# Optimization experiments

Hardware: AMD Instinct MI355X
Metric: run time of the kernel (lower is better)

The kernel has to match this reference:

```python
import jax, jax.numpy as jnp
import numpy as np
import math

B, C, L = 8, 128, 8192
MODES = 512
TIME_DIM = 256
HIDDEN = 352  # SwiGLU: int(2*4*128/3)=341 rounded up to multiple of 16
EPS = 1e-6


def setup_inputs() -> dict:
    key = jax.random.key(0)
    ks = jax.random.split(key, 16)
    scale = 1.0 / (C * C)
    return {
        "x": jax.random.normal(ks[0], (B, C, L), jnp.float32),
        "t_emb": jax.random.normal(ks[1], (B, TIME_DIM), jnp.float32),
        "w_real": scale * jax.random.normal(ks[2], (C, C, MODES), jnp.float32),
        "w_imag": scale * jax.random.normal(ks[3], (C, C, MODES), jnp.float32),
        "shifts": 0.05 * jax.random.normal(ks[4], (C,), jnp.float32),
        "pw_w": jax.random.normal(ks[5], (C, C), jnp.float32) / math.sqrt(C),
        "pw_b": jnp.zeros((C,), jnp.float32),
        "dw_w": jax.random.normal(ks[6], (C, 3), jnp.float32) / math.sqrt(3.0),
        "dw_b": jnp.zeros((C,), jnp.float32),
        "norm_w": jnp.ones((C,), jnp.float32),
        "w1": jax.random.normal(ks[7], (HIDDEN, C), jnp.float32) / math.sqrt(C),
        "w2": jax.random.normal(ks[8], (HIDDEN, C), jnp.float32) / math.sqrt(C),
        "w3": jax.random.normal(ks[9], (C, HIDDEN), jnp.float32) / math.sqrt(HIDDEN),
        "tw": jax.random.normal(ks[10], (C, TIME_DIM), jnp.float32) / math.sqrt(TIME_DIM),
        "tb": jnp.zeros((C,), jnp.float32),
    }


def reference(x, t_emb, w_real, w_imag, shifts, pw_w, pw_b, dw_w, dw_b,
              norm_w, w1, w2, w3, tw, tb):
    Lx = x.shape[-1]
    nfreq = Lx // 2 + 1
    k = min(MODES, nfreq)
    residual = x

    # --- spectral path ---
    x_ft = jnp.fft.rfft(x, axis=-1)  # (B,C,nfreq) complex64
    w = (w_real + 1j * w_imag)[:, :, :k]  # (C,O,modes)
    w_spec = jnp.einsum('bcm,com->bom', x_ft[:, :, :k], w)
    # SpectralRoPE phase rotation
    freqs = jnp.arange(MODES, dtype=jnp.float32)[:k]
    theta = -2.0 * jnp.pi * shifts[:, None] * freqs[None, :]  # (C,k)
    rot = jnp.exp(1j * theta)
    w_spec = w_spec * rot[None]
    out_ft = jnp.concatenate([w_spec, x_ft[:, :, k:]], axis=-1) if nfreq > k else w_spec
    global_out = jnp.fft.irfft(out_ft, n=Lx, axis=-1)

    # --- local path: pointwise (1x1) + depthwise (k=3, pad=1) conv ---
    pw = jnp.einsum('bcl,oc->bol', x, pw_w) + pw_b[None, :, None]
    xp = jnp.pad(x, ((0, 0), (0, 0), (1, 1)))
    dw = (dw_w[None, :, 0:1] * xp[:, :, :-2]
          + dw_w[None, :, 1:2] * xp[:, :, 1:-1]
          + dw_w[None, :, 2:3] * xp[:, :, 2:]) + dw_b[None, :, None]
    h = global_out + pw + dw

    # --- time bias ---
    t_bias = jax.nn.silu(t_emb) @ tw.T + tb  # (B,C)
    h = h + t_bias[:, :, None]

    # --- RMSNorm + SwiGLU over channel dim ---
    h = h.transpose(0, 2, 1)  # (B,L,C)
    h = h * jax.lax.rsqrt(jnp.mean(h * h, axis=-1, keepdims=True) + EPS)
    h = h * norm_w
    h = (jax.nn.silu(h @ w1.T) * (h @ w2.T)) @ w3.T
    h = h.transpose(0, 2, 1)  # (B,C,L)
    return h + residual
```

## Files before the change

### kernel.cpp

```cpp
#include <hip/hip_runtime.h>
#include <hip/hip_bf16.h>
#include <math.h>

typedef short short8 __attribute__((ext_vector_type(8)));
typedef short short4v __attribute__((ext_vector_type(4)));
typedef float f32x4 __attribute__((ext_vector_type(4)));
typedef __bf16 bf16x8 __attribute__((ext_vector_type(8)));

#define DEVI __device__ __forceinline__

DEVI float bf2f(short u) {
  union { unsigned int u32; float f; } c;
  c.u32 = ((unsigned int)(unsigned short)u) << 16;
  return c.f;
}
DEVI short f2bf(float f) {
  __hip_bfloat16 h = __float2bfloat16(f);
  unsigned short u;
  __builtin_memcpy(&u, &h, 2);
  return (short)u;
}
DEVI f32x4 mfma16(bf16x8 a, bf16x8 b, f32x4 c) {
  return __builtin_amdgcn_mfma_f32_16x16x32_bf16(a, b, c, 0, 0, 0);
}

#define GLL16(gsrc, ldst) __builtin_amdgcn_global_load_lds( \
    (__attribute__((address_space(1))) void*)(gsrc), \
    (__attribute__((address_space(3))) void*)(ldst), 16, 0, 0)

__global__ __launch_bounds__(256) void k_prep_x(const float* __restrict__ x,
                                                short* __restrict__ xbf,
                                                short* __restrict__ xT) {
  __shared__ short T[64][66];
  int t = threadIdx.x;
  int lt = blockIdx.x & 127;
  int ct = (blockIdx.x >> 7) & 1;
  int b  = blockIdx.x >> 8;
  int c0 = ct << 6, l0 = lt << 6;
  int i = t >> 2, j4 = (t & 3) << 4;
  const float* src = x + (size_t)(b * 128 + c0 + i) * 8192 + l0 + j4;
  short hv[16];
#pragma unroll
  for (int e = 0; e < 16; e += 4) {
    float4 v = *(const float4*)(src + e);
    hv[e] = f2bf(v.x); hv[e + 1] = f2bf(v.y); hv[e + 2] = f2bf(v.z); hv[e + 3] = f2bf(v.w);
  }
  short8 o0, o1;
#pragma unroll
  for (int e = 0; e < 8; ++e) { o0[e] = hv[e]; o1[e] = hv[8 + e]; }
  short* dst = xbf + (size_t)(b * 128 + c0 + i) * 8192 + l0 + j4;
  *(short8*)dst = o0;
  *(short8*)(dst + 8) = o1;
#pragma unroll
  for (int e = 0; e < 16; ++e) T[i][j4 + e] = hv[e];
  __syncthreads();
  int jj = t >> 2, i4 = (t & 3) << 4;
  short8 p0, p1;
#pragma unroll
  for (int e = 0; e < 8; ++e) { p0[e] = T[i4 + e][jj]; p1[e] = T[i4 + 8 + e][jj]; }
  short* d2 = xT + ((size_t)b * 8192 + l0 + jj) * 128 + c0 + i4;
  *(short8*)d2 = p0;
  *(short8*)(d2 + 8) = p1;
}

__global__ __launch_bounds__(256) void k_prep_tf(short* __restrict__ tf) {
  int n = blockIdx.x >> 2;
  int l0 = ((blockIdx.x & 3) << 11) + (threadIdx.x << 3);
  int m = n >> 1;
  int odd = n & 1;
  short8 o;
#pragma unroll
  for (int e = 0; e < 8; ++e) {
    int l = l0 + e;
    int r = (m * l) & 8191;
    float s, c;
    sincospif((float)r * (1.0f / 4096.0f), &s, &c);
    o[e] = f2bf(odd ? -s : c);
  }
  *(short8*)(tf + (size_t)n * 8192 + l0) = o;
}

__global__ __launch_bounds__(256) void k_prep_ti(short* __restrict__ ti) {
  int l = blockIdx.x;
  int k0 = threadIdx.x << 2;
  short4v o;
#pragma unroll
  for (int e = 0; e < 4; ++e) {
    int k = k0 + e;
    int m = (k < 512) ? k : (k - 512);
    int r = (m * l) & 8191;
    float s, c;
    sincospif((float)r * (1.0f / 4096.0f), &s, &c);
    o[e] = f2bf((k < 512) ? c : s);
  }
  *(short4v*)(ti + (size_t)l * 1024 + k0) = o;
}

__global__ __launch_bounds__(256) void k_prep_w(const float* __restrict__ w1,
                                                const float* __restrict__ w2,
                                                const float* __restrict__ w3,
                                                const float* __restrict__ pw_w,
                                                short* __restrict__ w12f,
                                                short* __restrict__ w3f,
                                                short* __restrict__ pwb) {
  int idx = blockIdx.x * 256 + threadIdx.x;
  if (idx < 98304) {
    int e = idx & 7, lane = (idx >> 3) & 63, ks = (idx >> 9) & 3, nt = idx >> 11;
    int rowk = lane & 15, kg = lane >> 4;
    int n = nt * 16 + rowk;
    int k = ks * 32 + kg * 8 + e;
    float v = 0.f;
    if (n < 352) v = w1[n * 128 + k];
    else if (n >= 384 && n < 736) v = w2[(n - 384) * 128 + k];
    w12f[idx] = f2bf(v);
  } else if (idx < 147456) {
    int q = idx - 98304;
    int e = q & 7, lane = (q >> 3) & 63;
    int rest = q >> 9;
    int nt = rest / 12, ks = rest - nt * 12;
    int rowk = lane & 15, kg = lane >> 4;
    int n = nt * 16 + rowk;
    int k = ks * 32 + kg * 8 + e;
    w3f[q] = f2bf(k < 352 ? w3[n * 352 + k] : 0.f);
  } else if (idx < 163840) {
    int q = idx - 147456;
    pwb[q] = f2bf(pw_w[q]);
  }
}

__global__ __launch_bounds__(256) void k_prep_bias(const float* __restrict__ t_emb,
                                                   const float* __restrict__ tw,
                                                   const float* __restrict__ tb,
                                                   const float* __restrict__ pw_b,
                                                   const float* __restrict__ dw_b,
                                                   float* __restrict__ bias) {
  __shared__ float s[256];
  int b = blockIdx.x, t = threadIdx.x;
  float v = t_emb[b * 256 + t];
  s[t] = v / (1.0f + __expf(-v));
  __syncthreads();
  if (t < 128) {
    float acc = tb[t] + pw_b[t] + dw_b[t];
    for (int j = 0; j < 256; ++j) acc += s[j] * tw[t * 256 + j];
    bias[b * 128 + t] = acc;
  }
}

__global__ __launch_bounds__(256) void k_zero(float4* __restrict__ p, int n4) {
  int i = blockIdx.x * 256 + threadIdx.x;
  if (i < n4) p[i] = make_float4(0.f, 0.f, 0.f, 0.f);
}

__global__ __launch_bounds__(256, 2) void k_fwd(const short* __restrict__ A,
                                                const short* __restrict__ Bt,
                                                float* __restrict__ X) {
  __shared__ short As[2][4096];
  __shared__ short Bs[2][4096];
  int t = threadIdx.x;
  int nt = blockIdx.x & 7;
  int mt = (blockIdx.x >> 3) & 7;
  int kc = blockIdx.x >> 6;
  int lane = t & 63, wv = t >> 6;
  int wr = wv >> 1, wc = wv & 1;

  int rA = t >> 2, g = t & 3;
  int gs0 = (g ^ ((rA >> 1) & 3)) << 3;
  int rB = rA + 64;
  int gs1 = (g ^ ((rB >> 1) & 3)) << 3;

  const short* aS0 = A + (size_t)(mt * 128 + rA) * 8192 + kc * 1024 + gs0;
  const short* aS1 = A + (size_t)(mt * 128 + rB) * 8192 + kc * 1024 + gs1;
  const short* bS0 = Bt + (size_t)(nt * 128 + rA) * 8192 + kc * 1024 + gs0;
  const short* bS1 = Bt + (size_t)(nt * 128 + rB) * 8192 + kc * 1024 + gs1;

  f32x4 acc[4][4];
#pragma unroll
  for (int i = 0; i < 4; ++i)
#pragma unroll
    for (int j = 0; j < 4; ++j) acc[i][j] = (f32x4){0.f, 0.f, 0.f, 0.f};

  GLL16(aS0, &As[0][t * 8]);
  GLL16(aS1, &As[0][2048 + t * 8]);
  GLL16(bS0, &Bs[0][t * 8]);
  GLL16(bS1, &Bs[0][2048 + t * 8]);

  int rowk = lane & 15, kg = lane >> 4;

  for (int ks = 0; ks < 32; ++ks) {
    __syncthreads();
    int buf = ks & 1;
    if (ks + 1 < 32) {
      int ko = (ks + 1) * 32;
      GLL16(aS0 + ko, &As[buf ^ 1][t * 8]);
      GLL16(aS1 + ko, &As[buf ^ 1][2048 + t * 8]);
      GLL16(bS0 + ko, &Bs[buf ^ 1][t * 8]);
      GLL16(bS1 + ko, &Bs[buf ^ 1][2048 + t * 8]);
    }
    bf16x8 af[4], bfr[4];
#pragma unroll
    for (int fr = 0; fr < 4; ++fr) {
      int rr = wr * 64 + fr * 16 + rowk;
      int gg = kg ^ ((rr >> 1) & 3);
      af[fr] = *(const bf16x8*)(&As[buf][rr * 32 + gg * 8]);
    }
#pragma unroll
    for (int fc = 0; fc < 4; ++fc) {
      int rr = wc * 64 + fc * 16 + rowk;
      int gg = kg ^ ((rr >> 1) & 3);
      bfr[fc] = *(const bf16x8*)(&Bs[buf][rr * 32 + gg * 8]);
    }
#pragma unroll
    for (int fr = 0; fr < 4; ++fr)
#pragma unroll
      for (int fc = 0; fc < 4; ++fc)
        acc[fr][fc] = mfma16(af[fr], bfr[fc], acc[fr][fc]);
  }

  int rbase = mt * 128 + wr * 64 + (lane >> 4) * 4;
  int cbase = nt * 128 + wc * 64 + (lane & 15);
#pragma unroll
  for (int fr = 0; fr < 4; ++fr)
#pragma unroll
    for (int fc = 0; fc < 4; ++fc)
#pragma unroll
      for (int j = 0; j < 4; ++j)
        unsafeAtomicAdd(&X[(size_t)(rbase + fr * 16 + j) * 1024 + cbase + fc * 16],
                        acc[fr][fc][j]);
}

__global__ __launch_bounds__(512) void k_spec(const float* __restrict__ X,
                                              const float* __restrict__ wre,
                                              const float* __restrict__ wim,
                                              const float* __restrict__ shifts,
                                              short* __restrict__ D) {
  __shared__ float red[16][256];
  int t = threadIdx.x;
  int tt = t & 255;
  int ch = t >> 8;
  int mt = blockIdx.x & 31, ot = blockIdx.x >> 5;
  int m = mt * 16 + (tt & 15);
  int o = ot * 16 + (tt >> 4);
  float ar[8], ai[8];
#pragma unroll
  for (int b = 0; b < 8; ++b) { ar[b] = 0.f; ai[b] = 0.f; }
  int cb = ch * 64;
  const float* wrp = wre + (size_t)(cb * 128 + o) * 512 + m;
  const float* wip = wim + (size_t)(cb * 128 + o) * 512 + m;
  const float* Xp = X + 2 * m;
#pragma unroll 4
  for (int cc = 0; cc < 64; ++cc) {
    float wr = wrp[(size_t)cc * 65536];
    float wi = wip[(size_t)cc * 65536];
    int c = cb + cc;
#pragma unroll
    for (int b = 0; b < 8; ++b) {
      float2 xv = *(const float2*)(Xp + (size_t)(b * 128 + c) * 1024);
      ar[b] += xv.x * wr - xv.y * wi;
      ai[b] += xv.x * wi + xv.y * wr;
    }
  }
  if (ch) {
#pragma unroll
    for (int b = 0; b < 8; ++b) { red[b * 2][tt] = ar[b]; red[b * 2 + 1][tt] = ai[b]; }
  }
  __syncthreads();
  if (!ch) {
#pragma unroll
    for (int b = 0; b < 8; ++b) { ar[b] += red[b * 2][tt]; ai[b] += red[b * 2 + 1][tt]; }
    float phi = -6.283185307179586f * shifts[o] * (float)m;
    float sp, cp;
    sincosf(phi, &sp, &cp);
    float sc = (m == 0 ? 1.0f : 2.0f) * (1.0f / 8192.0f);
#pragma unroll
    for (int b = 0; b < 8; ++b) {
      float yr = ar[b] * cp - ai[b] * sp;
      float yi = ar[b] * sp + ai[b] * cp;
      float2 xo = *(const float2*)(X + (size_t)(b * 128 + o) * 1024 + 2 * m);
      D[((size_t)b * 128 + o) * 1024 + m]       = f2bf(sc * (yr - xo.x));
      D[((size_t)b * 128 + o) * 1024 + 512 + m] = f2bf(-sc * (yi - xo.y));
    }
  }
}

__global__ __launch_bounds__(256, 2) void k_inv(const short* __restrict__ Ti,
                                                const short* __restrict__ D,
                                                const short* __restrict__ xT,
                                                const short* __restrict__ pwb,
                                                const float* __restrict__ dww,
                                                const float* __restrict__ bias,
                                                const float* __restrict__ nw,
                                                short* __restrict__ hn) {
  __shared__ short Sm[16384];
  __shared__ short xedge[256];
  __shared__ float rsS[2][128];
  short* As = Sm;
  short* Bs = Sm + 8192;
  int t = threadIdx.x;
  int lt = blockIdx.x & 63;
  int b  = blockIdx.x >> 6;
  int l0 = lt << 7;
  int lane = t & 63, wv = t >> 6;
  int wr = wv >> 1, wc = wv & 1;

  int rA = t >> 2, g = t & 3;
  int gs0 = (g ^ ((rA >> 1) & 3)) << 3;
  int rB = rA + 64;
  int gs1 = (g ^ ((rB >> 1) & 3)) << 3;

  const short* a1_0 = Ti + (size_t)(l0 + rA) * 1024 + gs0;
  const short* a1_1 = Ti + (size_t)(l0 + rB) * 1024 + gs1;
  const short* b1_0 = D + (size_t)(b * 128 + rA) * 1024 + gs0;
  const short* b1_1 = D + (size_t)(b * 128 + rB) * 1024 + gs1;
  const short* a2_0 = xT + ((size_t)b * 8192 + l0 + rA) * 128 + gs0;
  const short* a2_1 = xT + ((size_t)b * 8192 + l0 + rB) * 128 + gs1;
  const short* b2_0 = pwb + rA * 128 + gs0;
  const short* b2_1 = pwb + rB * 128 + gs1;

  f32x4 acc[4][4];
#pragma unroll
  for (int i = 0; i < 4; ++i)
#pragma unroll
    for (int j = 0; j < 4; ++j) acc[i][j] = (f32x4){0.f, 0.f, 0.f, 0.f};

  auto stage = [&](int buf, int ks) {
    int bo = buf * 4096;
    if (ks < 32) {
      int ko = ks * 32;
      GLL16(a1_0 + ko, &As[bo + t * 8]);
      GLL16(a1_1 + ko, &As[bo + 2048 + t * 8]);
      GLL16(b1_0 + ko, &Bs[bo + t * 8]);
      GLL16(b1_1 + ko, &Bs[bo + 2048 + t * 8]);
    } else {
      int ko = (ks - 32) * 32;
      GLL16(a2_0 + ko, &As[bo + t * 8]);
      GLL16(a2_1 + ko, &As[bo + 2048 + t * 8]);
      GLL16(b2_0 + ko, &Bs[bo + t * 8]);
      GLL16(b2_1 + ko, &Bs[bo + 2048 + t * 8]);
    }
  };

  stage(0, 0);
  int rowk = lane & 15, kg = lane >> 4;
  for (int ks = 0; ks < 36; ++ks) {
    __syncthreads();
    int buf = ks & 1;
    if (ks + 1 < 36) stage(buf ^ 1, ks + 1);
    bf16x8 af[4], bfr[4];
#pragma unroll
    for (int fr = 0; fr < 4; ++fr) {
      int rr = wr * 64 + fr * 16 + rowk;
      int gg = kg ^ ((rr >> 1) & 3);
      af[fr] = *(const bf16x8*)(&As[buf * 4096 + rr * 32 + gg * 8]);
    }
#pragma unroll
    for (int fc = 0; fc < 4; ++fc) {
      int rr = wc * 64 + fc * 16 + rowk;
      int gg = kg ^ ((rr >> 1) & 3);
      bfr[fc] = *(const bf16x8*)(&Bs[buf * 4096 + rr * 32 + gg * 8]);
    }
#pragma unroll
    for (int fr = 0; fr < 4; ++fr)
#pragma unroll
      for (int fc = 0; fc < 4; ++fc)
        acc[fr][fc] = mfma16(af[fr], bfr[fc], acc[fr][fc]);
  }

  __syncthreads();
  for (int i = t; i < 2080; i += 256) {
    if (i < 2048) {
      int row = i >> 4, seg = i & 15;
      short8 v = *(const short8*)(xT + ((size_t)b * 8192 + l0 + row) * 128 + seg * 8);
      *(short8*)(&Sm[row * 128 + seg * 8]) = v;
    } else {
      int e2 = i - 2048;
      int which = e2 >> 4, seg = e2 & 15;
      int l = which ? (l0 + 128) : (l0 - 1);
      short8 v = {0, 0, 0, 0, 0, 0, 0, 0};
      if (l >= 0 && l < 8192)
        v = *(const short8*)(xT + ((size_t)b * 8192 + l) * 128 + seg * 8);
      *(short8*)(&xedge[which * 128 + seg * 8]) = v;
    }
  }
  __syncthreads();

  const float* bb = bias + b * 128;
#pragma unroll
  for (int fc = 0; fc < 4; ++fc) {
    int o = wc * 64 + fc * 16 + rowk;
    float w0 = dww[o * 3], w1v = dww[o * 3 + 1], w2v = dww[o * 3 + 2];
    float bo = bb[o];
#pragma unroll
    for (int fr = 0; fr < 4; ++fr) {
#pragma unroll
      for (int j = 0; j < 4; ++j) {
        int ll = wr * 64 + fr * 16 + kg * 4 + j;
        float xm = (ll == 0)   ? bf2f(xedge[o])       : bf2f(Sm[(ll - 1) * 128 + o]);
        float x0 = bf2f(Sm[ll * 128 + o]);
        float xp = (ll == 127) ? bf2f(xedge[128 + o]) : bf2f(Sm[(ll + 1) * 128 + o]);
        acc[fr][fc][j] += w0 * xm + w1v * x0 + w2v * xp + bo + x0;
      }
    }
  }
#pragma unroll
  for (int fr = 0; fr < 4; ++fr) {
#pragma unroll
    for (int j = 0; j < 4; ++j) {
      float s = 0.f;
#pragma unroll
      for (int fc = 0; fc < 4; ++fc) { float v = acc[fr][fc][j]; s += v * v; }
      s += __shfl_xor(s, 1);
      s += __shfl_xor(s, 2);
      s += __shfl_xor(s, 4);
      s += __shfl_xor(s, 8);
      if (rowk == 0) rsS[wc][wr * 64 + fr * 16 + kg * 4 + j] = s;
    }
  }
  __syncthreads();
#pragma unroll
  for (int fr = 0; fr < 4; ++fr) {
#pragma unroll
    for (int j = 0; j < 4; ++j) {
      int ll = wr * 64 + fr * 16 + kg * 4 + j;
      float rms = rsqrtf((rsS[0][ll] + rsS[1][ll]) * (1.0f / 128.0f) + 1e-6f);
#pragma unroll
      for (int fc = 0; fc < 4; ++fc) {
        int o = wc * 64 + fc * 16 + rowk;
        hn[((size_t)b * 8192 + l0 + ll) * 128 + o] = f2bf(acc[fr][fc][j] * rms * nw[o]);
      }
    }
  }
}

__global__ __launch_bounds__(512, 2) void k_swi(const short* __restrict__ hn,
                                                const short* __restrict__ w12f,
                                                const short* __restrict__ w3f,
                                                const float* __restrict__ x,
                                                float* __restrict__ out) {
  __shared__ short smem[32768];
  short* hA = smem;
  short* uA = smem + 8192;
  float* tr = (float*)smem;

  int t = threadIdx.x;
  int lane = t & 63, wv = t >> 6;
  int rb = blockIdx.x;
  int bb_ = rb >> 7;
  int l0 = (rb & 127) << 6;
  size_t row0 = (size_t)rb * 64;

#pragma unroll
  for (int c = 0; c < 2; ++c) {
    int sidx = (wv * 2 + c) * 512 + lane * 8;
    int row = sidx >> 7;
    int g = (sidx >> 3) & 15;
    const short* src = hn + (row0 + row) * 128 + (g ^ (row & 7)) * 8;
    GLL16(src, &hA[sidx]);
  }
  __syncthreads();

  int wr = wv >> 2, wq = wv & 3;
  int rowk = lane & 15, kg = lane >> 4;

  f32x4 acc1[2][6], acc2[2][6];
#pragma unroll
  for (int i = 0; i < 2; ++i)
#pragma unroll
    for (int j = 0; j < 6; ++j) {
      acc1[i][j] = (f32x4){0.f, 0.f, 0.f, 0.f};
      acc2[i][j] = (f32x4){0.f, 0.f, 0.f, 0.f};
    }
#pragma unroll
  for (int ks = 0; ks < 4; ++ks) {
    bf16x8 a[2];
#pragma unroll
    for (int fr = 0; fr < 2; ++fr) {
      int rr = wr * 32 + fr * 16 + rowk;
      int gg = (ks * 4 + kg) ^ (rr & 7);
      a[fr] = *(const bf16x8*)(&hA[rr * 128 + gg * 8]);
    }
#pragma unroll
    for (int fc = 0; fc < 6; ++fc) {
      int nt = wq * 6 + fc;
      bf16x8 b1 = *(const bf16x8*)(w12f + ((size_t)(nt * 4 + ks) * 64 + lane) * 8);
      bf16x8 b2 = *(const bf16x8*)(w12f + ((size_t)((nt + 24) * 4 + ks) * 64 + lane) * 8);
#pragma unroll
      for (int fr = 0; fr < 2; ++fr) {
        acc1[fr][fc] = mfma16(a[fr], b1, acc1[fr][fc]);
        acc2[fr][fc] = mfma16(a[fr], b2, acc2[fr][fc]);
      }
    }
  }
#pragma unroll
  for (int fr = 0; fr < 2; ++fr)
#pragma unroll
    for (int fc = 0; fc < 6; ++fc)
#pragma unroll
      for (int j = 0; j < 4; ++j) {
        float a1 = acc1[fr][fc][j], a2 = acc2[fr][fc][j];
        float u = a1 / (1.f + __expf(-a1)) * a2;
        int row = wr * 32 + fr * 16 + kg * 4 + j;
        int col = wq * 96 + fc * 16 + rowk;
        int cg = (col >> 3) ^ (row & 7);
        uA[row * 384 + cg * 8 + (col & 7)] = f2bf(u);
      }
  __syncthreads();

  f32x4 acc[2][2];
#pragma unroll
  for (int i = 0; i < 2; ++i)
#pragma unroll
    for (int j = 0; j < 2; ++j) acc[i][j] = (f32x4){0.f, 0.f, 0.f, 0.f};
#pragma unroll
  for (int ks = 0; ks < 12; ++ks) {
    bf16x8 a[2];
#pragma unroll
    for (int fr = 0; fr < 2; ++fr) {
      int rr = wr * 32 + fr * 16 + rowk;
      int gg = (ks * 4 + kg) ^ (rr & 7);
      a[fr] = *(const bf16x8*)(&uA[rr * 384 + gg * 8]);
    }
#pragma unroll
    for (int fc = 0; fc < 2; ++fc) {
      int nt = wq * 2 + fc;
      bf16x8 bw = *(const bf16x8*)(w3f + ((size_t)(nt * 12 + ks) * 64 + lane) * 8);
#pragma unroll
      for (int fr = 0; fr < 2; ++fr) acc[fr][fc] = mfma16(a[fr], bw, acc[fr][fc]);
    }
  }
  __syncthreads();
#pragma unroll
  for (int fr = 0; fr < 2; ++fr)
#pragma unroll
    for (int fc = 0; fc < 2; ++fc)
#pragma unroll
      for (int j = 0; j < 4; ++j) {
        int r = wr * 32 + fr * 16 + kg * 4 + j;
        int c = wq * 32 + fc * 16 + rowk;
        tr[c * 65 + r] = acc[fr][fc][j];
      }
  __syncthreads();
  {
    int o = t >> 2, q = t & 3;
    const float* xs = x + ((size_t)(bb_ * 128 + o)) * 8192 + l0 + q * 16;
    float* os = out + ((size_t)(bb_ * 128 + o)) * 8192 + l0 + q * 16;
#pragma unroll
    for (int e4 = 0; e4 < 4; ++e4) {
      float4 xv = *(const float4*)(xs + e4 * 4);
      float4 r;
      r.x = tr[o * 65 + q * 16 + e4 * 4 + 0] + xv.x;
      r.y = tr[o * 65 + q * 16 + e4 * 4 + 1] + xv.y;
      r.z = tr[o * 65 + q * 16 + e4 * 4 + 2] + xv.z;
      r.w = tr[o * 65 + q * 16 + e4 * 4 + 3] + xv.w;
      *(float4*)(os + e4 * 4) = r;
    }
  }
}

extern "C" void kernel_launch(void* const* d_in, const int* in_sizes, int n_in,
                              void* d_out, int out_size, void* d_ws, size_t ws_size,
                              hipStream_t stream) {
  const float* x      = (const float*)d_in[0];
  const float* t_emb  = (const float*)d_in[1];
  const float* w_real = (const float*)d_in[2];
  const float* w_imag = (const float*)d_in[3];
  const float* shifts = (const float*)d_in[4];
  const float* pw_w   = (const float*)d_in[5];
  const float* pw_b   = (const float*)d_in[6];
  const float* dw_w   = (const float*)d_in[7];
  const float* dw_b   = (const float*)d_in[8];
  const float* norm_w = (const float*)d_in[9];
  const float* w1     = (const float*)d_in[10];
  const float* w2     = (const float*)d_in[11];
  const float* w3     = (const float*)d_in[12];
  const float* tw     = (const float*)d_in[13];
  const float* tb     = (const float*)d_in[14];
  float* out = (float*)d_out;
  char* ws = (char*)d_ws;

  short* xbf  = (short*)(ws + 0);
  short* xT   = (short*)(ws + 16777216);
  short* tf   = (short*)(ws + 33554432);
  short* ti   = (short*)(ws + 50331648);
  float* Xb   = (float*)(ws + 67108864);
  short* Db   = (short*)(ws + 71303168);
  short* hn   = (short*)(ws + 73400320);
  short* w12f = (short*)(ws + 90177536);
  short* w3f  = (short*)(ws + 90374144);
  short* pwb  = (short*)(ws + 90472448);
  float* bias = (float*)(ws + 90505216);

  k_prep_x<<<2048, 256, 0, stream>>>(x, xbf, xT);
  k_prep_tf<<<4096, 256, 0, stream>>>(tf);
  k_prep_ti<<<8192, 256, 0, stream>>>(ti);
  k_prep_w<<<640, 256, 0, stream>>>(w1, w2, w3, pw_w, w12f, w3f, pwb);
  k_prep_bias<<<8, 256, 0, stream>>>(t_emb, tw, tb, pw_b, dw_b, bias);
  k_zero<<<1024, 256, 0, stream>>>((float4*)Xb, 262144);
  k_fwd<<<512, 256, 0, stream>>>(xbf, tf, Xb);
  k_spec<<<256, 512, 0, stream>>>(Xb, w_real, w_imag, shifts, Db);
  k_inv<<<512, 256, 0, stream>>>(ti, Db, xT, pwb, dw_w, bias, norm_w, hn);
  k_swi<<<1024, 512, 0, stream>>>(hn, w12f, w3f, x, out);
}
```

Baseline: 404.8 us.

## Triple-buffer LDS with explicit vmcnt waits in GEMM kernels; stage hn stores via LDS

The forward and inverse GEMM kernels move from double to triple LDS buffering, prefetching two k-steps ahead. The per-step __syncthreads is replaced by raw s_barrier plus explicit s_waitcnt vmcnt counts, so global loads stay in flight across iterations. Launch bounds rise to 3 blocks per CU. The k_inv epilogue now writes normalized bf16 output to LDS first and then stores it with coalesced 16-byte writes instead of scattered 2-byte stores. This costs more shared memory per block and relies on hand-tuned vmcnt counts matching the number of outstanding loads.

```diff
diff --git a/kernel.cpp b/kernel.cpp
--- a/kernel.cpp
+++ b/kernel.cpp
@@ -151,11 +151,11 @@
   if (i < n4) p[i] = make_float4(0.f, 0.f, 0.f, 0.f);
 }
 
-__global__ __launch_bounds__(256, 2) void k_fwd(const short* __restrict__ A,
+__global__ __launch_bounds__(256, 3) void k_fwd(const short* __restrict__ A,
                                                 const short* __restrict__ Bt,
                                                 float* __restrict__ X) {
-  __shared__ short As[2][4096];
-  __shared__ short Bs[2][4096];
+  __shared__ short As[12288];
+  __shared__ short Bs[12288];
   int t = threadIdx.x;
   int nt = blockIdx.x & 7;
   int mt = (blockIdx.x >> 3) & 7;
@@ -179,35 +179,41 @@
 #pragma unroll
     for (int j = 0; j < 4; ++j) acc[i][j] = (f32x4){0.f, 0.f, 0.f, 0.f};
 
-  GLL16(aS0, &As[0][t * 8]);
-  GLL16(aS1, &As[0][2048 + t * 8]);
-  GLL16(bS0, &Bs[0][t * 8]);
-  GLL16(bS1, &Bs[0][2048 + t * 8]);
+  auto stage = [&](int p, int ks) {
+    int ao = p * 4096;
+    int ko = ks * 32;
+    GLL16(aS0 + ko, &As[ao + t * 8]);
+    GLL16(aS1 + ko, &As[ao + 2048 + t * 8]);
+    GLL16(bS0 + ko, &Bs[ao + t * 8]);
+    GLL16(bS1 + ko, &Bs[ao + 2048 + t * 8]);
+  };
+
+  stage(0, 0);
+  stage(1, 1);
 
   int rowk = lane & 15, kg = lane >> 4;
 
   for (int ks = 0; ks < 32; ++ks) {
-    __syncthreads();
-    int buf = ks & 1;
-    if (ks + 1 < 32) {
-      int ko = (ks + 1) * 32;
-      GLL16(aS0 + ko, &As[buf ^ 1][t * 8]);
-      GLL16(aS1 + ko, &As[buf ^ 1][2048 + t * 8]);
-      GLL16(bS0 + ko, &Bs[buf ^ 1][t * 8]);
-      GLL16(bS1 + ko, &Bs[buf ^ 1][2048 + t * 8]);
-    }
+    int p = ks % 3;
+    __builtin_amdgcn_s_barrier();
+    if (ks + 2 < 32) stage((ks + 2) % 3, ks + 2);
+    if (ks < 30)      { asm volatile("s_waitcnt vmcnt(8)" ::: "memory"); }
+    else if (ks == 30){ asm volatile("s_waitcnt vmcnt(4)" ::: "memory"); }
+    else              { asm volatile("s_waitcnt vmcnt(0)" ::: "memory"); }
+    __builtin_amdgcn_s_barrier();
+    __builtin_amdgcn_sched_barrier(0);
     bf16x8 af[4], bfr[4];
 #pragma unroll
     for (int fr = 0; fr < 4; ++fr) {
       int rr = wr * 64 + fr * 16 + rowk;
       int gg = kg ^ ((rr >> 1) & 3);
-      af[fr] = *(const bf16x8*)(&As[buf][rr * 32 + gg * 8]);
+      af[fr] = *(const bf16x8*)(&As[p * 4096 + rr * 32 + gg * 8]);
     }
 #pragma unroll
     for (int fc = 0; fc < 4; ++fc) {
       int rr = wc * 64 + fc * 16 + rowk;
       int gg = kg ^ ((rr >> 1) & 3);
-      bfr[fc] = *(const bf16x8*)(&Bs[buf][rr * 32 + gg * 8]);
+      bfr[fc] = *(const bf16x8*)(&Bs[p * 4096 + rr * 32 + gg * 8]);
     }
 #pragma unroll
     for (int fr = 0; fr < 4; ++fr)
@@ -282,7 +288,7 @@
   }
 }
 
-__global__ __launch_bounds__(256, 2) void k_inv(const short* __restrict__ Ti,
+__global__ __launch_bounds__(256, 3) void k_inv(const short* __restrict__ Ti,
                                                 const short* __restrict__ D,
                                                 const short* __restrict__ xT,
                                                 const short* __restrict__ pwb,
@@ -290,11 +296,9 @@
                                                 const float* __restrict__ bias,
                                                 const float* __restrict__ nw,
                                                 short* __restrict__ hn) {
-  __shared__ short Sm[16384];
+  __shared__ short Sm[24576];
   __shared__ short xedge[256];
   __shared__ float rsS[2][128];
-  short* As = Sm;
-  short* Bs = Sm + 8192;
   int t = threadIdx.x;
   int lt = blockIdx.x & 63;
   int b  = blockIdx.x >> 6;
@@ -322,41 +326,49 @@
 #pragma unroll
     for (int j = 0; j < 4; ++j) acc[i][j] = (f32x4){0.f, 0.f, 0.f, 0.f};
 
-  auto stage = [&](int buf, int ks) {
-    int bo = buf * 4096;
+  auto stage = [&](int p, int ks) {
+    int ao = p * 4096;
+    int bo = 12288 + p * 4096;
     if (ks < 32) {
       int ko = ks * 32;
-      GLL16(a1_0 + ko, &As[bo + t * 8]);
-      GLL16(a1_1 + ko, &As[bo + 2048 + t * 8]);
-      GLL16(b1_0 + ko, &Bs[bo + t * 8]);
-      GLL16(b1_1 + ko, &Bs[bo + 2048 + t * 8]);
+      GLL16(a1_0 + ko, &Sm[ao + t * 8]);
+      GLL16(a1_1 + ko, &Sm[ao + 2048 + t * 8]);
+      GLL16(b1_0 + ko, &Sm[bo + t * 8]);
+      GLL16(b1_1 + ko, &Sm[bo + 2048 + t * 8]);
     } else {
       int ko = (ks - 32) * 32;
-      GLL16(a2_0 + ko, &As[bo + t * 8]);
-      GLL16(a2_1 + ko, &As[bo + 2048 + t * 8]);
-      GLL16(b2_0 + ko, &Bs[bo + t * 8]);
-      GLL16(b2_1 + ko, &Bs[bo + 2048 + t * 8]);
+      GLL16(a2_0 + ko, &Sm[ao + t * 8]);
+      GLL16(a2_1 + ko, &Sm[ao + 2048 + t * 8]);
+      GLL16(b2_0 + ko, &Sm[bo + t * 8]);
+      GLL16(b2_1 + ko, &Sm[bo + 2048 + t * 8]);
     }
   };
 
   stage(0, 0);
+  stage(1, 1);
+
   int rowk = lane & 15, kg = lane >> 4;
   for (int ks = 0; ks < 36; ++ks) {
-    __syncthreads();
-    int buf = ks & 1;
-    if (ks + 1 < 36) stage(buf ^ 1, ks + 1);
+    int p = ks % 3;
+    __builtin_amdgcn_s_barrier();
+    if (ks + 2 < 36) stage((ks + 2) % 3, ks + 2);
+    if (ks < 34)      { asm volatile("s_waitcnt vmcnt(8)" ::: "memory"); }
+    else if (ks == 34){ asm volatile("s_waitcnt vmcnt(4)" ::: "memory"); }
+    else              { asm volatile("s_waitcnt vmcnt(0)" ::: "memory"); }
+    __builtin_amdgcn_s_barrier();
+    __builtin_amdgcn_sched_barrier(0);
     bf16x8 af[4], bfr[4];
 #pragma unroll
     for (int fr = 0; fr < 4; ++fr) {
       int rr = wr * 64 + fr * 16 + rowk;
       int gg = kg ^ ((rr >> 1) & 3);
-      af[fr] = *(const bf16x8*)(&As[buf * 4096 + rr * 32 + gg * 8]);
+      af[fr] = *(const bf16x8*)(&Sm[p * 4096 + rr * 32 + gg * 8]);
     }
 #pragma unroll
     for (int fc = 0; fc < 4; ++fc) {
       int rr = wc * 64 + fc * 16 + rowk;
       int gg = kg ^ ((rr >> 1) & 3);
-      bfr[fc] = *(const bf16x8*)(&Bs[buf * 4096 + rr * 32 + gg * 8]);
+      bfr[fc] = *(const bf16x8*)(&Sm[12288 + p * 4096 + rr * 32 + gg * 8]);
     }
 #pragma unroll
     for (int fr = 0; fr < 4; ++fr)
@@ -425,8 +437,18 @@
 #pragma unroll
       for (int fc = 0; fc < 4; ++fc) {
         int o = wc * 64 + fc * 16 + rowk;
-        hn[((size_t)b * 8192 + l0 + ll) * 128 + o] = f2bf(acc[fr][fc][j] * rms * nw[o]);
+        Sm[ll * 128 + o] = f2bf(acc[fr][fc][j] * rms * nw[o]);
       }
+    }
+  }
+  __syncthreads();
+  {
+    size_t rb = (size_t)b * 8192 + l0;
+#pragma unroll
+    for (int it = 0; it < 8; ++it) {
+      int idx = it * 256 + t;
+      int row = idx >> 4, seg = idx & 15;
+      *(short8*)(hn + (rb + row) * 128 + seg * 8) = *(const short8*)(&Sm[row * 128 + seg * 8]);
     }
   }
 }
```

Measured after the change: 416.3 us. +2.8%, slower.
